# Performance work log

Hardware: AMD Instinct MI355X
Metric: run time of the kernel (lower is better)

## Reference

```python
import jax, jax.numpy as jnp
import numpy as np

N_LEVELS = 16
F = 2
LOG2_T = 19
T = 1 << LOG2_T
BASE_RES = 16.0
FINEST_RES = 512.0
N_SAMPLES = 128
NEAR, FAR = 2.0, 6.0
BOX_MIN = jnp.array([-1.5, -1.5, -1.5], jnp.float32)
BOX_MAX = jnp.array([1.5, 1.5, 1.5], jnp.float32)
GEO_FEAT = 15
OUT_CH = 4

_PRIMES = np.array([1, 2654435761, 805459861], dtype=np.uint32)
_OFFSETS = np.array([[i, j, k] for i in (0, 1) for j in (0, 1) for k in (0, 1)], dtype=np.int32)  # [8,3]
_B = np.exp((np.log(FINEST_RES) - np.log(BASE_RES)) / (N_LEVELS - 1))
_RESOLUTIONS = np.floor(BASE_RES * _B ** np.arange(N_LEVELS)).astype(np.float32)


def setup_inputs() -> dict:
    key = jax.random.key(0)
    ks = jax.random.split(key, 10)
    n_rays = 16384
    o = jax.random.uniform(ks[0], (n_rays, 3), jnp.float32, -0.5, 0.5)
    d = jax.random.normal(ks[1], (n_rays, 3), jnp.float32)
    d = d / jnp.linalg.norm(d, axis=-1, keepdims=True)
    rays = jnp.concatenate([o, d], -1)
    hash_tables = jax.random.uniform(ks[2], (N_LEVELS, T, F), jnp.float32, -1e-4, 1e-4)
    def w(k, di, do):
        return jax.random.normal(k, (di, do), jnp.float32) * (1.0 / np.sqrt(di))
    return dict(
        rays=rays,
        hash_tables=hash_tables,
        ws0=w(ks[3], 32, 64), ws1=w(ks[4], 64, 64), ws2=w(ks[5], 64, 1 + GEO_FEAT),
        wc0=w(ks[6], 16 + GEO_FEAT, 64), wc1=w(ks[7], 64, 64), wc2=w(ks[8], 64, 64), wc3=w(ks[9], 64, OUT_CH - 1),
    )


def _hash_embed(x, tables):
    """Multi-res hash grid: x [P,3] world coords, tables [L,T,F] -> ([P,L*F], keep_mask [P])."""
    xc = jnp.clip(x, BOX_MIN, BOX_MAX)
    keep = jnp.all(x == xc, axis=-1)
    offs = jnp.asarray(_OFFSETS)          # [8,3]
    primes = jnp.asarray(_PRIMES)         # uint32
    feats = []
    for l in range(N_LEVELS):
        grid = (BOX_MAX - BOX_MIN) / _RESOLUTIONS[l]
        bl = jnp.floor((xc - BOX_MIN) / grid).astype(jnp.int32)   # [P,3] bottom-left voxel index
        vmin = bl.astype(jnp.float32) * grid + BOX_MIN
        wts = (xc - vmin) / grid                                  # trilinear weights [P,3]
        corners = (bl[:, None, :] + offs[None]).astype(jnp.uint32)  # [P,8,3]
        h = (corners[..., 0] * primes[0]) ^ (corners[..., 1] * primes[1]) ^ (corners[..., 2] * primes[2])
        idx = (h & jnp.uint32(T - 1)).astype(jnp.int32)           # [P,8]
        e = tables[l][idx]                                        # [P,8,F]
        w0, w1, w2 = wts[:, 0:1], wts[:, 1:2], wts[:, 2:3]
        c00 = e[:, 0] * (1 - w0) + e[:, 4] * w0
        c01 = e[:, 1] * (1 - w0) + e[:, 5] * w0
        c10 = e[:, 2] * (1 - w0) + e[:, 6] * w0
        c11 = e[:, 3] * (1 - w0) + e[:, 7] * w0
        c0 = c00 * (1 - w1) + c10 * w1
        c1 = c01 * (1 - w1) + c11 * w1
        feats.append(c0 * (1 - w2) + c1 * w2)
    return jnp.concatenate(feats, -1), keep


def _sh_encode(d):
    """Degree-4 spherical harmonics encoding, [P,3] -> [P,16]."""
    x, y, z = d[..., 0], d[..., 1], d[..., 2]
    xx, yy, zz = x * x, y * y, z * z
    xy, yz, xz = x * y, y * z, x * z
    C0 = 0.28209479177387814
    C1 = 0.4886025119029199
    C2 = (1.0925484305920792, -1.0925484305920792, 0.31539156525252005, -1.0925484305920792, 0.5462742152960396)
    C3 = (-0.5900435899266435, 2.890611442640554, -0.4570457994644658, 0.3731763325901154,
          -0.4570457994644658, 1.445305721320277, -0.5900435899266435)
    return jnp.stack([
        jnp.full_like(x, C0),
        -C1 * y, C1 * z, -C1 * x,
        C2[0] * xy, C2[1] * yz, C2[2] * (2.0 * zz - xx - yy), C2[3] * xz, C2[4] * (xx - yy),
        C3[0] * y * (3.0 * xx - yy), C3[1] * xy * z, C3[2] * y * (4.0 * zz - xx - yy),
        C3[3] * z * (2.0 * zz - 3.0 * xx - 3.0 * yy), C3[4] * x * (4.0 * zz - xx - yy),
        C3[5] * z * (xx - yy), C3[6] * x * (xx - 3.0 * yy),
    ], axis=-1)


def _forward(rays, hash_tables, ws0, ws1, ws2, wc0, wc1, wc2, wc3):
    n_rays = rays.shape[0]
    o, d = rays[:, :3], rays[:, 3:6]
    z = jnp.linspace(NEAR, FAR, N_SAMPLES, dtype=jnp.float32)
    zvals = jnp.broadcast_to(z, (n_rays, N_SAMPLES))
    pts = o[:, None, :] + d[:, None, :] * z[None, :, None]       # [N,S,3]
    P = n_rays * N_SAMPLES
    pts_f = pts.reshape(P, 3)
    dirs_f = jnp.broadcast_to(d[:, None, :], (n_rays, N_SAMPLES, 3)).reshape(P, 3)

    enc_pts, keep = _hash_embed(pts_f, hash_tables)              # [P,32], [P]
    enc_dirs = _sh_encode(dirs_f)                                # [P,16]

    # NeRFSmall: bias-free sigma net then color net
    h = jnp.maximum(enc_pts @ ws0, 0.0)
    h = jnp.maximum(h @ ws1, 0.0)
    h = h @ ws2                                                   # [P, 1+GEO_FEAT]
    sigma, geo = h[:, 0], h[:, 1:]
    hc = jnp.concatenate([enc_dirs, geo], -1)
    hc = jnp.maximum(hc @ wc0, 0.0)
    hc = jnp.maximum(hc @ wc1, 0.0)
    hc = jnp.maximum(hc @ wc2, 0.0)
    color = hc @ wc3                                              # [P, OUT_CH-1]

    sigma = jnp.where(keep, sigma, 0.0)                           # output[~keep_mask, -1] = 0
    raw = jnp.concatenate([color, sigma[:, None]], -1).reshape(n_rays, N_SAMPLES, OUT_CH)

    # Integrator (raw2outputs)
    dists = zvals[:, 1:] - zvals[:, :-1]
    dists = jnp.concatenate([dists, jnp.full((n_rays, 1), 1e10, jnp.float32)], -1)
    dists = dists * jnp.linalg.norm(d, axis=-1, keepdims=True)
    chs = jax.nn.sigmoid(raw[..., :-1])
    alpha = 1.0 - jnp.exp(-jnp.maximum(raw[..., -1], 0.0) * dists)
    trans = jnp.cumprod(1.0 - alpha + 1e-10, axis=-1)
    trans = jnp.concatenate([jnp.ones((n_rays, 1), jnp.float32), trans[:, :-1]], -1)
    weights = alpha * trans
    chs_map = jnp.einsum('ns,nsc->nc', weights, chs)
    depth_map = jnp.sum(weights * zvals, -1)
    probs = jnp.concatenate([weights, 1.0 - jnp.sum(weights, -1, keepdims=True) + 1e-6], -1)
    p = probs / jnp.sum(probs, -1, keepdims=True)
    sparsity_loss = -jnp.sum(p * jnp.log(jnp.clip(p, 1e-37)), -1)
    return chs_map, depth_map, sparsity_loss


def reference(rays, hash_tables, ws0, ws1, ws2, wc0, wc1, wc2, wc3):
    return _forward(rays, hash_tables, ws0, ws1, ws2, wc0, wc1, wc2, wc3)
```

## Files before the change

kernel.cpp:

```cpp
#include <hip/hip_runtime.h>

#define NRAYS 16384
#define NLEV  16
#define THASH 524288
#define MAXACT 48
#define MAXPTS (NRAYS*MAXACT)
#define MBLK  256
#define MGRID 1024
#define STR   68

__device__ __forceinline__ float zval32(int i) {
  const float step = 4.0f / 127.0f;
  return __fadd_rn(2.0f, __fmul_rn((float)i, step));
}
__device__ __forceinline__ float pcoord(float o, float d, float z) {
  return __fadd_rn(o, __fmul_rn(d, z));
}

__global__ __launch_bounds__(64)
void k_classify(const float* __restrict__ rays,
                float* __restrict__ sh,
                unsigned* __restrict__ counter,
                unsigned* __restrict__ rbase,
                unsigned* __restrict__ rn,
                unsigned* __restrict__ plist) {
  int lane = threadIdx.x;
  int r = blockIdx.x * 64 + lane;
  if (r >= NRAYS) return;
  float ox = rays[6*r+0], oy = rays[6*r+1], oz = rays[6*r+2];
  float dx = rays[6*r+3], dy = rays[6*r+4], dz = rays[6*r+5];
  float x = dx, y = dy, z = dz;
  float xx = x*x, yy = y*y, zz = z*z, xy = x*y, yz = y*z, xz = x*z;
  float* shp = sh + 16*r;
  shp[0]  = 0.28209479177387814f;
  shp[1]  = -0.4886025119029199f * y;
  shp[2]  =  0.4886025119029199f * z;
  shp[3]  = -0.4886025119029199f * x;
  shp[4]  =  1.0925484305920792f * xy;
  shp[5]  = -1.0925484305920792f * yz;
  shp[6]  =  0.31539156525252005f * (2.0f*zz - xx - yy);
  shp[7]  = -1.0925484305920792f * xz;
  shp[8]  =  0.5462742152960396f * (xx - yy);
  shp[9]  = -0.5900435899266435f * y * (3.0f*xx - yy);
  shp[10] =  2.890611442640554f  * xy * z;
  shp[11] = -0.4570457994644658f * y * (4.0f*zz - xx - yy);
  shp[12] =  0.3731763325901154f * z * (2.0f*zz - 3.0f*xx - 3.0f*yy);
  shp[13] = -0.4570457994644658f * x * (4.0f*zz - xx - yy);
  shp[14] =  1.445305721320277f  * z * (xx - yy);
  shp[15] = -0.5900435899266435f * x * (xx - 3.0f*yy);
  unsigned n = 0;
  for (int i = 0; i < 128; ++i) {
    float zi = zval32(i);
    float px = pcoord(ox, dx, zi);
    float py = pcoord(oy, dy, zi);
    float pz = pcoord(oz, dz, zi);
    bool in = (px >= -1.5f) && (px <= 1.5f) && (py >= -1.5f) && (py <= 1.5f)
           && (pz >= -1.5f) && (pz <= 1.5f);
    if (!in) break;
    ++n;
  }
  unsigned pre = n;
#pragma unroll
  for (int d = 1; d < 64; d <<= 1) {
    unsigned v = __shfl_up(pre, d, 64);
    if (lane >= d) pre += v;
  }
  unsigned excl  = pre - n;
  unsigned total = __shfl(pre, 63, 64);
  unsigned base0 = 0;
  if (lane == 0) base0 = atomicAdd(counter, total);
  base0 = __shfl(base0, 0, 64);
  unsigned base = base0 + excl;
  rbase[r] = base;
  rn[r]    = n;
  for (unsigned i = 0; i < n; ++i) plist[base + i] = (unsigned)(r*128 + (int)i);
}

template<int IN, int TOTOUT, bool RELU>
__device__ __forceinline__ void layerT(const float* __restrict__ W,
                                       const float* __restrict__ Ain,
                                       float* __restrict__ Bout,
                                       int lane, int pb) {
  if (lane < TOTOUT) {
    float acc[16];
#pragma unroll
    for (int p = 0; p < 16; ++p) acc[p] = 0.0f;
#pragma unroll 2
    for (int k = 0; k < IN; ++k) {
      float w = W[k*TOTOUT + lane];
      const float4* ar = (const float4*)(Ain + k*STR + pb);
      float4 a0 = ar[0], a1 = ar[1], a2 = ar[2], a3 = ar[3];
      acc[ 0] = fmaf(w, a0.x, acc[ 0]); acc[ 1] = fmaf(w, a0.y, acc[ 1]);
      acc[ 2] = fmaf(w, a0.z, acc[ 2]); acc[ 3] = fmaf(w, a0.w, acc[ 3]);
      acc[ 4] = fmaf(w, a1.x, acc[ 4]); acc[ 5] = fmaf(w, a1.y, acc[ 5]);
      acc[ 6] = fmaf(w, a1.z, acc[ 6]); acc[ 7] = fmaf(w, a1.w, acc[ 7]);
      acc[ 8] = fmaf(w, a2.x, acc[ 8]); acc[ 9] = fmaf(w, a2.y, acc[ 9]);
      acc[10] = fmaf(w, a2.z, acc[10]); acc[11] = fmaf(w, a2.w, acc[11]);
      acc[12] = fmaf(w, a3.x, acc[12]); acc[13] = fmaf(w, a3.y, acc[13]);
      acc[14] = fmaf(w, a3.z, acc[14]); acc[15] = fmaf(w, a3.w, acc[15]);
    }
    float4* br = (float4*)(Bout + lane*STR + pb);
#pragma unroll
    for (int c = 0; c < 4; ++c) {
      float4 v;
      v.x = RELU ? fmaxf(acc[4*c+0], 0.0f) : acc[4*c+0];
      v.y = RELU ? fmaxf(acc[4*c+1], 0.0f) : acc[4*c+1];
      v.z = RELU ? fmaxf(acc[4*c+2], 0.0f) : acc[4*c+2];
      v.w = RELU ? fmaxf(acc[4*c+3], 0.0f) : acc[4*c+3];
      br[c] = v;
    }
  }
}

__global__ __launch_bounds__(MBLK, 4)
void k_mlp(const float* __restrict__ rays,
           const float* __restrict__ tables,
           const float* __restrict__ w_s0, const float* __restrict__ w_s1,
           const float* __restrict__ w_s2, const float* __restrict__ w_c0,
           const float* __restrict__ w_c1, const float* __restrict__ w_c2,
           const float* __restrict__ w_c3,
           const float* __restrict__ sh,
           const unsigned* __restrict__ counter,
           const unsigned* __restrict__ plist,
           float4* __restrict__ results) {
  __shared__ __align__(16) float A[64*STR];
  __shared__ __align__(16) float B[64*STR];
  __shared__ float sig_s[64];
  const int t = threadIdx.x;
  const int lane = t & 63;
  const int q = __builtin_amdgcn_readfirstlane(t >> 6);
  const int pb = q*16;
  const unsigned count = *counter;
  const unsigned ntiles = (count + 63u) >> 6;
  const float RESF[NLEV] = {16.f,20.f,25.f,32.f,40.f,50.f,64.f,80.f,
                            101.f,128.f,161.f,203.f,256.f,322.f,406.f,512.f};
  for (unsigned tile = blockIdx.x; tile < ntiles; tile += MGRID) {
    unsigned s = (tile << 6) + (unsigned)lane;
    unsigned pid = (s < count) ? plist[s] : 0u;
    int r = (int)(pid >> 7);
    int i = (int)(pid & 127u);
    {
      float zi = zval32(i);
      float px = pcoord(rays[6*r+0], rays[6*r+3], zi);
      float py = pcoord(rays[6*r+1], rays[6*r+4], zi);
      float pz = pcoord(rays[6*r+2], rays[6*r+5], zi);
      float xcx = fminf(fmaxf(px, -1.5f), 1.5f);
      float xcy = fminf(fmaxf(py, -1.5f), 1.5f);
      float xcz = fminf(fmaxf(pz, -1.5f), 1.5f);
#pragma unroll
      for (int li = 0; li < 4; ++li) {
        int l = 4*q + li;
        const float grid = 3.0f / RESF[l];
        float bfx = floorf(__fdiv_rn(__fadd_rn(xcx, 1.5f), grid));
        float bfy = floorf(__fdiv_rn(__fadd_rn(xcy, 1.5f), grid));
        float bfz = floorf(__fdiv_rn(__fadd_rn(xcz, 1.5f), grid));
        float vmx = __fadd_rn(__fmul_rn(bfx, grid), -1.5f);
        float vmy = __fadd_rn(__fmul_rn(bfy, grid), -1.5f);
        float vmz = __fadd_rn(__fmul_rn(bfz, grid), -1.5f);
        float wx = __fdiv_rn(__fsub_rn(xcx, vmx), grid);
        float wy = __fdiv_rn(__fsub_rn(xcy, vmy), grid);
        float wz = __fdiv_rn(__fsub_rn(xcz, vmz), grid);
        unsigned cx0 = (unsigned)(int)bfx, cy0 = (unsigned)(int)bfy, cz0 = (unsigned)(int)bfz;
        unsigned cx1 = cx0 + 1u, cy1 = cy0 + 1u, cz1 = cz0 + 1u;
        unsigned hy0 = cy0*2654435761u, hy1 = cy1*2654435761u;
        unsigned hz0 = cz0*805459861u,  hz1 = cz1*805459861u;
        const float2* tb = (const float2*)tables + (size_t)l*THASH;
        float2 e000 = tb[(cx0^hy0^hz0)&(THASH-1)];
        float2 e001 = tb[(cx0^hy0^hz1)&(THASH-1)];
        float2 e010 = tb[(cx0^hy1^hz0)&(THASH-1)];
        float2 e011 = tb[(cx0^hy1^hz1)&(THASH-1)];
        float2 e100 = tb[(cx1^hy0^hz0)&(THASH-1)];
        float2 e101 = tb[(cx1^hy0^hz1)&(THASH-1)];
        float2 e110 = tb[(cx1^hy1^hz0)&(THASH-1)];
        float2 e111 = tb[(cx1^hy1^hz1)&(THASH-1)];
        float iwx = 1.f-wx, iwy = 1.f-wy, iwz = 1.f-wz;
        float c00a = e000.x*iwx + e100.x*wx, c00b = e000.y*iwx + e100.y*wx;
        float c01a = e001.x*iwx + e101.x*wx, c01b = e001.y*iwx + e101.y*wx;
        float c10a = e010.x*iwx + e110.x*wx, c10b = e010.y*iwx + e110.y*wx;
        float c11a = e011.x*iwx + e111.x*wx, c11b = e011.y*iwx + e111.y*wx;
        float c0a = c00a*iwy + c10a*wy, c0b = c00b*iwy + c10b*wy;
        float c1a = c01a*iwy + c11a*wy, c1b = c01b*iwy + c11b*wy;
        A[(2*l+0)*STR + lane] = c0a*iwz + c1a*wz;
        A[(2*l+1)*STR + lane] = c0b*iwz + c1b*wz;
      }
    }
    __syncthreads();
    layerT<32,64,true >(w_s0, A, B, lane, pb); __syncthreads();
    layerT<64,64,true >(w_s1, B, A, lane, pb); __syncthreads();
    layerT<64,16,false>(w_s2, A, B, lane, pb); __syncthreads();
    if (t < 64) sig_s[t] = B[0*STR + t];
    for (int idx = t; idx < 31*64; idx += MBLK) {
      int k = idx >> 6, p = idx & 63;
      float v;
      if (k < 16) {
        unsigned sp = (tile << 6) + (unsigned)p;
        unsigned pp = (sp < count) ? plist[sp] : 0u;
        v = sh[(pp >> 7)*16 + k];
      } else {
        v = B[(k-15)*STR + p];
      }
      A[k*STR + p] = v;
    }
    __syncthreads();
    layerT<31,64,true >(w_c0, A, B, lane, pb); __syncthreads();
    layerT<64,64,true >(w_c1, B, A, lane, pb); __syncthreads();
    layerT<64,64,true >(w_c2, A, B, lane, pb); __syncthreads();
    layerT<64, 3,false>(w_c3, B, A, lane, pb);
    __syncthreads();
    if (lane < 16) {
      int p = pb + lane;
      unsigned ss = (tile << 6) + (unsigned)p;
      if (ss < count) {
        float4 res;
        res.x = sig_s[p];
        res.y = A[0*STR + p];
        res.z = A[1*STR + p];
        res.w = A[2*STR + p];
        results[ss] = res;
      }
    }
    __syncthreads();
  }
}

__global__ __launch_bounds__(64)
void k_comp(const float* __restrict__ rays,
            const unsigned* __restrict__ rbase,
            const unsigned* __restrict__ rn,
            const float4* __restrict__ results,
            float* __restrict__ out) {
  int r = blockIdx.x * 64 + threadIdx.x;
  if (r >= NRAYS) return;
  float dx = rays[6*r+3], dy = rays[6*r+4], dz = rays[6*r+5];
  float dnorm = sqrtf(dx*dx + dy*dy + dz*dz);
  int n = (int)rn[r];
  unsigned base = rbase[r];
  const float step = 4.0f/127.0f;
  const float diststep = __fmul_rn(step, dnorm);
  float S = 0.f, ch0 = 0.f, ch1 = 0.f, ch2 = 0.f, dep = 0.f, trans = 1.f;
  for (int i = 0; i < n; ++i) {
    float4 rs = results[base + i];
    float z = zval32(i);
    float sg = fmaxf(rs.x, 0.f);
    float alpha = -expm1f(-__fmul_rn(sg, diststep));
    float w = __fmul_rn(alpha, trans);
    trans = __fmul_rn(trans, __fadd_rn(__fsub_rn(1.f, alpha), 1e-10f));
    float s0 = 1.f/(1.f + expf(-rs.y));
    float s1 = 1.f/(1.f + expf(-rs.z));
    float s2 = 1.f/(1.f + expf(-rs.w));
    S += w; ch0 += w*s0; ch1 += w*s1; ch2 += w*s2; dep += w*z;
  }
  float rem  = __fadd_rn(__fsub_rn(1.f, S), 1e-6f);
  float Stot = __fadd_rn(S, rem);
  float loss = 0.f, trans2 = 1.f;
  for (int i = 0; i < n; ++i) {
    float4 rs = results[base + i];
    float sg = fmaxf(rs.x, 0.f);
    float alpha = -expm1f(-__fmul_rn(sg, diststep));
    float w = __fmul_rn(alpha, trans2);
    trans2 = __fmul_rn(trans2, __fadd_rn(__fsub_rn(1.f, alpha), 1e-10f));
    float p = __fdiv_rn(w, Stot);
    loss += p * logf(fmaxf(p, 1e-37f));
  }
  float pl = __fdiv_rn(rem, Stot);
  loss += pl * logf(fmaxf(pl, 1e-37f));
  out[3*r+0] = ch0; out[3*r+1] = ch1; out[3*r+2] = ch2;
  out[3*NRAYS + r] = dep;
  out[4*NRAYS + r] = -loss;
}

extern "C" void kernel_launch(void* const* d_in, const int* in_sizes, int n_in,
                              void* d_out, int out_size, void* d_ws, size_t ws_size,
                              hipStream_t stream) {
  const float* rays   = (const float*)d_in[0];
  const float* tables = (const float*)d_in[1];
  const float* ws0    = (const float*)d_in[2];
  const float* ws1    = (const float*)d_in[3];
  const float* ws2    = (const float*)d_in[4];
  const float* wc0    = (const float*)d_in[5];
  const float* wc1    = (const float*)d_in[6];
  const float* wc2    = (const float*)d_in[7];
  const float* wc3    = (const float*)d_in[8];

  char* ws = (char*)d_ws;
  unsigned* counter = (unsigned*)ws;
  unsigned* rbase   = (unsigned*)(ws + 256);
  unsigned* rn      = (unsigned*)(ws + 256 + 65536);
  float*    sh      = (float*)  (ws + 256 + 131072);
  float4*   results = (float4*) (ws + 1179904);
  unsigned* plist   = (unsigned*)(ws + 1179904 + (size_t)MAXPTS*16);

  hipMemsetAsync(counter, 0, 4, stream);
  k_classify<<<NRAYS/64, 64, 0, stream>>>(rays, sh, counter, rbase, rn, plist);
  k_mlp<<<MGRID, MBLK, 0, stream>>>(rays, tables, ws0, ws1, ws2,
                                    wc0, wc1, wc2, wc3, sh, counter, plist, results);
  k_comp<<<NRAYS/64, 64, 0, stream>>>(rays, rbase, rn, results, (float*)d_out);
}
```

Measured before the change: 218.0 us.

## Make MLP tiles wave-local with point-major rows to drop block barriers

Each wavefront now owns 16 points, and its four 16-lane groups split the output neurons. Activations are stored point-major per row in LDS, so every layer is computed and consumed inside one wave and all the __syncthreads between layers go away. Weights are read as float4 loads from global, broadcast across each lane group. The last two small layers get dedicated routines, and results are written directly without a shared sigma buffer. The min-blocks occupancy hint is also relaxed. In exchange, the code relies on wave-lockstep LDS visibility, and the per-lane row reads with stride 68 may cause bank conflicts.

Result: slower. 251.6 us (+15.4%).

```diff
diff --git a/kernel.cpp b/kernel.cpp
--- a/kernel.cpp
+++ b/kernel.cpp
@@ -76,43 +76,95 @@
   for (unsigned i = 0; i < n; ++i) plist[base + i] = (unsigned)(r*128 + (int)i);
 }
 
-template<int IN, int TOTOUT, bool RELU>
-__device__ __forceinline__ void layerT(const float* __restrict__ W,
+#define FMAC16(a_, Wp_)                                                     \
+  { const float4* __restrict__ Wk = (const float4*)(Wp_);                   \
+    float4 w0 = Wk[0], w1 = Wk[1], w2 = Wk[2], w3 = Wk[3];                  \
+    acc[ 0]=fmaf(a_,w0.x,acc[ 0]); acc[ 1]=fmaf(a_,w0.y,acc[ 1]);           \
+    acc[ 2]=fmaf(a_,w0.z,acc[ 2]); acc[ 3]=fmaf(a_,w0.w,acc[ 3]);           \
+    acc[ 4]=fmaf(a_,w1.x,acc[ 4]); acc[ 5]=fmaf(a_,w1.y,acc[ 5]);           \
+    acc[ 6]=fmaf(a_,w1.z,acc[ 6]); acc[ 7]=fmaf(a_,w1.w,acc[ 7]);           \
+    acc[ 8]=fmaf(a_,w2.x,acc[ 8]); acc[ 9]=fmaf(a_,w2.y,acc[ 9]);           \
+    acc[10]=fmaf(a_,w2.z,acc[10]); acc[11]=fmaf(a_,w2.w,acc[11]);           \
+    acc[12]=fmaf(a_,w3.x,acc[12]); acc[13]=fmaf(a_,w3.y,acc[13]);           \
+    acc[14]=fmaf(a_,w3.z,acc[14]); acc[15]=fmaf(a_,w3.w,acc[15]); }
+
+template<int IN, bool RELU>
+__device__ __forceinline__ void layer64(const float* __restrict__ W,
+                                        const float* __restrict__ Ain,
+                                        float* __restrict__ Bout,
+                                        int row, int jb) {
+  float acc[16];
+#pragma unroll
+  for (int j = 0; j < 16; ++j) acc[j] = 0.0f;
+  const float4* __restrict__ Arow = (const float4*)(Ain + row);
+#pragma unroll 2
+  for (int g = 0; g < IN/4; ++g) {
+    float4 a4 = Arow[g];
+    FMAC16(a4.x, W + (4*g+0)*64 + jb);
+    FMAC16(a4.y, W + (4*g+1)*64 + jb);
+    FMAC16(a4.z, W + (4*g+2)*64 + jb);
+    FMAC16(a4.w, W + (4*g+3)*64 + jb);
+  }
+#pragma unroll
+  for (int k = (IN & ~3); k < IN; ++k) {
+    float a = Ain[row + k];
+    FMAC16(a, W + k*64 + jb);
+  }
+  float4* __restrict__ Brow = (float4*)(Bout + row + jb);
+#pragma unroll
+  for (int c = 0; c < 4; ++c) {
+    float4 v;
+    v.x = RELU ? fmaxf(acc[4*c+0], 0.0f) : acc[4*c+0];
+    v.y = RELU ? fmaxf(acc[4*c+1], 0.0f) : acc[4*c+1];
+    v.z = RELU ? fmaxf(acc[4*c+2], 0.0f) : acc[4*c+2];
+    v.w = RELU ? fmaxf(acc[4*c+3], 0.0f) : acc[4*c+3];
+    Brow[c] = v;
+  }
+}
+
+__device__ __forceinline__ float layer16(const float* __restrict__ W,
+                                         const float* __restrict__ Ain,
+                                         float* __restrict__ Bout,
+                                         int row, int jb4) {
+  float acc[4] = {0.f, 0.f, 0.f, 0.f};
+  const float4* __restrict__ Arow = (const float4*)(Ain + row);
+#pragma unroll 4
+  for (int g = 0; g < 16; ++g) {
+    float4 a4 = Arow[g];
+#pragma unroll
+    for (int ks = 0; ks < 4; ++ks) {
+      int k = 4*g + ks;
+      float a = (ks==0)?a4.x:(ks==1)?a4.y:(ks==2)?a4.z:a4.w;
+      float4 w = *(const float4*)(W + k*16 + jb4);
+      acc[0]=fmaf(a,w.x,acc[0]); acc[1]=fmaf(a,w.y,acc[1]);
+      acc[2]=fmaf(a,w.z,acc[2]); acc[3]=fmaf(a,w.w,acc[3]);
+    }
+  }
+  *(float4*)(Bout + row + jb4) = make_float4(acc[0],acc[1],acc[2],acc[3]);
+  return acc[0];
+}
+
+__device__ __forceinline__ void layer3(const float* __restrict__ W,
                                        const float* __restrict__ Ain,
-                                       float* __restrict__ Bout,
-                                       int lane, int pb) {
-  if (lane < TOTOUT) {
-    float acc[16];
-#pragma unroll
-    for (int p = 0; p < 16; ++p) acc[p] = 0.0f;
-#pragma unroll 2
-    for (int k = 0; k < IN; ++k) {
-      float w = W[k*TOTOUT + lane];
-      const float4* ar = (const float4*)(Ain + k*STR + pb);
-      float4 a0 = ar[0], a1 = ar[1], a2 = ar[2], a3 = ar[3];
-      acc[ 0] = fmaf(w, a0.x, acc[ 0]); acc[ 1] = fmaf(w, a0.y, acc[ 1]);
-      acc[ 2] = fmaf(w, a0.z, acc[ 2]); acc[ 3] = fmaf(w, a0.w, acc[ 3]);
-      acc[ 4] = fmaf(w, a1.x, acc[ 4]); acc[ 5] = fmaf(w, a1.y, acc[ 5]);
-      acc[ 6] = fmaf(w, a1.z, acc[ 6]); acc[ 7] = fmaf(w, a1.w, acc[ 7]);
-      acc[ 8] = fmaf(w, a2.x, acc[ 8]); acc[ 9] = fmaf(w, a2.y, acc[ 9]);
-      acc[10] = fmaf(w, a2.z, acc[10]); acc[11] = fmaf(w, a2.w, acc[11]);
-      acc[12] = fmaf(w, a3.x, acc[12]); acc[13] = fmaf(w, a3.y, acc[13]);
-      acc[14] = fmaf(w, a3.z, acc[14]); acc[15] = fmaf(w, a3.w, acc[15]);
-    }
-    float4* br = (float4*)(Bout + lane*STR + pb);
-#pragma unroll
-    for (int c = 0; c < 4; ++c) {
-      float4 v;
-      v.x = RELU ? fmaxf(acc[4*c+0], 0.0f) : acc[4*c+0];
-      v.y = RELU ? fmaxf(acc[4*c+1], 0.0f) : acc[4*c+1];
-      v.z = RELU ? fmaxf(acc[4*c+2], 0.0f) : acc[4*c+2];
-      v.w = RELU ? fmaxf(acc[4*c+3], 0.0f) : acc[4*c+3];
-      br[c] = v;
-    }
-  }
-}
-
-__global__ __launch_bounds__(MBLK, 4)
+                                       int row, float out3[3]) {
+  float a0 = 0.f, a1 = 0.f, a2 = 0.f;
+  const float4* __restrict__ Arow = (const float4*)(Ain + row);
+#pragma unroll 4
+  for (int g = 0; g < 16; ++g) {
+    float4 a4 = Arow[g];
+#pragma unroll
+    for (int ks = 0; ks < 4; ++ks) {
+      int k = 4*g + ks;
+      float a = (ks==0)?a4.x:(ks==1)?a4.y:(ks==2)?a4.z:a4.w;
+      a0 = fmaf(a, W[k*3+0], a0);
+      a1 = fmaf(a, W[k*3+1], a1);
+      a2 = fmaf(a, W[k*3+2], a2);
+    }
+  }
+  out3[0]=a0; out3[1]=a1; out3[2]=a2;
+}
+
+__global__ __launch_bounds__(MBLK)
 void k_mlp(const float* __restrict__ rays,
            const float* __restrict__ tables,
            const float* __restrict__ w_s0, const float* __restrict__ w_s1,
@@ -125,17 +177,23 @@
            float4* __restrict__ results) {
   __shared__ __align__(16) float A[64*STR];
   __shared__ __align__(16) float B[64*STR];
-  __shared__ float sig_s[64];
   const int t = threadIdx.x;
   const int lane = t & 63;
-  const int q = __builtin_amdgcn_readfirstlane(t >> 6);
-  const int pb = q*16;
+  const int p    = lane & 15;
+  const int jg   = lane >> 4;
+  const int q    = __builtin_amdgcn_readfirstlane(t >> 6);
+  const int wb   = q * 16;
+  const int gp   = wb + p;
+  const int row  = gp * STR;
+  const int jb   = jg * 16;
+  int zoff = 0; asm volatile("" : "+v"(zoff));
+  const float* __restrict__ w_c3v = w_c3 + zoff;
   const unsigned count = *counter;
   const unsigned ntiles = (count + 63u) >> 6;
   const float RESF[NLEV] = {16.f,20.f,25.f,32.f,40.f,50.f,64.f,80.f,
                             101.f,128.f,161.f,203.f,256.f,322.f,406.f,512.f};
   for (unsigned tile = blockIdx.x; tile < ntiles; tile += MGRID) {
-    unsigned s = (tile << 6) + (unsigned)lane;
+    unsigned s = (tile << 6) + (unsigned)gp;
     unsigned pid = (s < count) ? plist[s] : 0u;
     int r = (int)(pid >> 7);
     int i = (int)(pid & 127u);
@@ -149,7 +207,7 @@
       float xcz = fminf(fmaxf(pz, -1.5f), 1.5f);
 #pragma unroll
       for (int li = 0; li < 4; ++li) {
-        int l = 4*q + li;
+        int l = 4*jg + li;
         const float grid = 3.0f / RESF[l];
         float bfx = floorf(__fdiv_rn(__fadd_rn(xcx, 1.5f), grid));
         float bfy = floorf(__fdiv_rn(__fadd_rn(xcy, 1.5f), grid));
@@ -180,46 +238,31 @@
         float c11a = e011.x*iwx + e111.x*wx, c11b = e011.y*iwx + e111.y*wx;
         float c0a = c00a*iwy + c10a*wy, c0b = c00b*iwy + c10b*wy;
         float c1a = c01a*iwy + c11a*wy, c1b = c01b*iwy + c11b*wy;
-        A[(2*l+0)*STR + lane] = c0a*iwz + c1a*wz;
-        A[(2*l+1)*STR + lane] = c0b*iwz + c1b*wz;
+        float2 f2;
+        f2.x = c0a*iwz + c1a*wz;
+        f2.y = c0b*iwz + c1b*wz;
+        *(float2*)(A + row + 2*l) = f2;
       }
     }
-    __syncthreads();
-    layerT<32,64,true >(w_s0, A, B, lane, pb); __syncthreads();
-    layerT<64,64,true >(w_s1, B, A, lane, pb); __syncthreads();
-    layerT<64,16,false>(w_s2, A, B, lane, pb); __syncthreads();
-    if (t < 64) sig_s[t] = B[0*STR + t];
-    for (int idx = t; idx < 31*64; idx += MBLK) {
-      int k = idx >> 6, p = idx & 63;
-      float v;
-      if (k < 16) {
-        unsigned sp = (tile << 6) + (unsigned)p;
-        unsigned pp = (sp < count) ? plist[sp] : 0u;
-        v = sh[(pp >> 7)*16 + k];
-      } else {
-        v = B[(k-15)*STR + p];
+    layer64<32,true >(w_s0, A, B, row, jb);
+    layer64<64,true >(w_s1, B, A, row, jb);
+    float sigma_r = layer16(w_s2, A, B, row, jg*4);
+    {
+      const float* shp = sh + r*16;
+      int k0 = jg*8, k1 = (jg==3) ? 31 : (k0+8);
+      for (int k = k0; k < k1; ++k) {
+        float v = (k < 16) ? shp[k] : B[row + (k-15)];
+        A[row + k] = v;
       }
-      A[k*STR + p] = v;
-    }
-    __syncthreads();
-    layerT<31,64,true >(w_c0, A, B, lane, pb); __syncthreads();
-    layerT<64,64,true >(w_c1, B, A, lane, pb); __syncthreads();
-    layerT<64,64,true >(w_c2, A, B, lane, pb); __syncthreads();
-    layerT<64, 3,false>(w_c3, B, A, lane, pb);
-    __syncthreads();
-    if (lane < 16) {
-      int p = pb + lane;
-      unsigned ss = (tile << 6) + (unsigned)p;
-      if (ss < count) {
-        float4 res;
-        res.x = sig_s[p];
-        res.y = A[0*STR + p];
-        res.z = A[1*STR + p];
-        res.w = A[2*STR + p];
-        results[ss] = res;
-      }
-    }
-    __syncthreads();
+    }
+    layer64<31,true >(w_c0, A, B, row, jb);
+    layer64<64,true >(w_c1, B, A, row, jb);
+    layer64<64,true >(w_c2, A, B, row, jb);
+    float c3o[3];
+    layer3(w_c3v, B, row, c3o);
+    if (jg == 0 && s < count) {
+      results[s] = make_float4(sigma_r, c3o[0], c3o[1], c3o[2]);
+    }
   }
 }
 
@@ -259,8 +302,8 @@
     float alpha = -expm1f(-__fmul_rn(sg, diststep));
     float w = __fmul_rn(alpha, trans2);
     trans2 = __fmul_rn(trans2, __fadd_rn(__fsub_rn(1.f, alpha), 1e-10f));
-    float p = __fdiv_rn(w, Stot);
-    loss += p * logf(fmaxf(p, 1e-37f));
+    float pq = __fdiv_rn(w, Stot);
+    loss += pq * logf(fmaxf(pq, 1e-37f));
   }
   float pl = __fdiv_rn(rem, Stot);
   loss += pl * logf(fmaxf(pl, 1e-37f));
```
